# Optimization experiments

Measured on AMD Instinct MI355X. Metric: run time of the kernel, lower is better.

## Reference

```python
import jax, jax.numpy as jnp
import numpy as np

N, E, IN_DIM, H, EDGE_DIM, T, SCALE = 50000, 800000, 16, 32, 4, 4, 3

def setup_inputs() -> dict:
    key = jax.random.key(0)
    ks = jax.random.split(key, 12)
    s = 0.1
    return {
        "inputs": jax.random.normal(ks[0], (N, IN_DIM), jnp.float32),
        "e_feats": jax.random.normal(ks[1], (E, EDGE_DIM, T), jnp.float32),
        "rain0": jax.random.uniform(ks[2], (N, T), jnp.float32),
        "W_emb": jax.random.normal(ks[3], (IN_DIM, H), jnp.float32) * s,
        "W_edge_in": jax.random.normal(ks[4], (SCALE - 1, H + EDGE_DIM, H), jnp.float32) * s,
        "W_node_in": jax.random.normal(ks[5], (SCALE - 1, 2 * H + 1, H), jnp.float32) * s,
        "W_edge_out": jax.random.normal(ks[6], (H + EDGE_DIM, H), jnp.float32) * s,
        "W_node_out": jax.random.normal(ks[7], (2 * H + 1, H), jnp.float32) * s,
        "W_rain": jax.random.normal(ks[8], (H, 1), jnp.float32) * s,
        "src": jax.random.randint(ks[9], (E,), 0, N, jnp.int32),
        "dst": jax.random.randint(ks[10], (E,), 0, N, jnp.int32),
    }


def _eiconv(h, ef, rain, W_e, W_n, src, dst):
    # edge-conditioned message: act_edge(W_e @ [h_src ; e_feat])  -> [E, H]
    m = jax.nn.relu(jnp.concatenate([h[src], ef], axis=-1) @ W_e)
    # scatter-sum to destination nodes  -> [N, H]
    agg = jax.ops.segment_sum(m, dst, num_segments=h.shape[0])
    # node update conditioned on rain driver: act_o(W_n @ [h ; agg ; rain])
    return jax.nn.relu(jnp.concatenate([h, agg, rain[:, None]], axis=-1) @ W_n)


def reference(inputs, e_feats, rain0, W_emb, W_edge_in, W_node_in, W_edge_out, W_node_out, W_rain, src, dst):
    h0 = inputs @ W_emb  # embedding, no bias  [N, H]
    ef_t = jnp.transpose(e_feats, (2, 0, 1))  # [T, E, edge_dim]
    rain_t = rain0.T  # [T, N]

    def step(h, xs):
        ef, rain = xs
        for s in range(SCALE - 1):  # IN layers (fixed small loop)
            h = _eiconv(h, ef, rain, W_edge_in[s], W_node_in[s], src, dst)
        h = _eiconv(h, ef, rain, W_edge_out, W_node_out, src, dst)  # OUT layer
        r = (h @ W_rain)[:, 0]  # per-node rain scalar
        return h, r

    _, rains = jax.lax.scan(step, h0, (ef_t, rain_t))  # rains: [T, N]
    return rains.T  # rain_all: [N, T]
```

## Files before the change

kernel.cpp:

```cpp
#include <hip/hip_runtime.h>
#include <cstdint>

#define NN 50000
#define NE 800000
#define IN_DIM 16
#define H 32
#define EDGE_DIM 4
#define T_STEPS 4
#define NPB 32
#define NBLK ((NN + NPB - 1) / NPB)
#define SBLK 196

typedef __bf16 bf16x8 __attribute__((ext_vector_type(8)));
typedef float f32x4 __attribute__((ext_vector_type(4)));
typedef unsigned int u32x4 __attribute__((ext_vector_type(4)));

__device__ __forceinline__ uint32_t bf_rne1(float f) {
    uint32_t u = __float_as_uint(f);
    return (u + 0x7FFFu + ((u >> 16) & 1u)) >> 16;
}
__device__ __forceinline__ float bf2f(uint32_t h16) { return __uint_as_float(h16 << 16); }
__device__ __forceinline__ uint32_t bfpair(float a, float b) {
    return (bf_rne1(b) << 16) | bf_rne1(a);
}
__device__ __forceinline__ bf16x8 asbf(u32x4 u) { return __builtin_bit_cast(bf16x8, u); }
__device__ __forceinline__ f32x4 MFMA(bf16x8 a, bf16x8 b, f32x4 c) {
    return __builtin_amdgcn_mfma_f32_16x16x32_bf16(a, b, c, 0, 0, 0);
}

__device__ __forceinline__ void store_hpk(uint32_t* hpk, int n, int cq, float4 a) {
    int off = (cq & 3) * 4 + (cq >> 2) * 2;
    uint32_t p0 = bfpair(a.x, a.y), p1 = bfpair(a.z, a.w);
    *(uint2*)(hpk + (size_t)n * 32 + off) = make_uint2(p0, p1);
    float r0 = a.x - bf2f(p0 & 0xFFFFu), r1 = a.y - bf2f(p0 >> 16);
    float r2 = a.z - bf2f(p1 & 0xFFFFu), r3 = a.w - bf2f(p1 >> 16);
    *(uint2*)(hpk + (size_t)n * 32 + 16 + off) = make_uint2(bfpair(r0, r1), bfpair(r2, r3));
}

__global__ __launch_bounds__(256) void embed_kernel(const float* __restrict__ inputs,
                                                    const float* __restrict__ W_emb,
                                                    float* __restrict__ h,
                                                    uint32_t* __restrict__ hpk) {
    int idx = blockIdx.x * 256 + threadIdx.x;
    if (idx >= NN * 8) return;
    int n = idx >> 3, cq = idx & 7;
    const float* xr = inputs + (size_t)n * IN_DIM;
    float4 a = make_float4(0.f, 0.f, 0.f, 0.f);
#pragma unroll
    for (int k = 0; k < IN_DIM; ++k) {
        float xk = xr[k];
        float4 w = *(const float4*)(W_emb + k * 32 + cq * 4);
        a.x = fmaf(xk, w.x, a.x); a.y = fmaf(xk, w.y, a.y);
        a.z = fmaf(xk, w.z, a.z); a.w = fmaf(xk, w.w, a.w);
    }
    *(float4*)(h + (size_t)n * 32 + cq * 4) = a;
    store_hpk(hpk, n, cq, a);
}

__global__ __launch_bounds__(256) void hist_kernel(const int* __restrict__ dst, int* __restrict__ deg) {
    int e = blockIdx.x * 256 + threadIdx.x;
    if (e < NE) atomicAdd(&deg[dst[e]], 1);
}

__global__ __launch_bounds__(256) void scan_part(const int* __restrict__ deg, int* __restrict__ bsum) {
    __shared__ int red[256];
    int i = blockIdx.x * 256 + threadIdx.x;
    red[threadIdx.x] = (i < NN) ? deg[i] : 0;
    __syncthreads();
    for (int off = 128; off > 0; off >>= 1) {
        if (threadIdx.x < off) red[threadIdx.x] += red[threadIdx.x + off];
        __syncthreads();
    }
    if (threadIdx.x == 0) bsum[blockIdx.x] = red[0];
}

__global__ __launch_bounds__(256) void scan_tops(const int* __restrict__ bsum, int* __restrict__ btop) {
    __shared__ int s[256];
    int tid = threadIdx.x;
    int v0 = (tid < SBLK) ? bsum[tid] : 0;
    s[tid] = v0;
    __syncthreads();
    for (int off = 1; off < 256; off <<= 1) {
        int v = (tid >= off) ? s[tid - off] : 0;
        __syncthreads();
        s[tid] += v;
        __syncthreads();
    }
    if (tid < SBLK) btop[tid] = s[tid] - v0;
}

__global__ __launch_bounds__(256) void scan_final(const int* __restrict__ deg,
                                                  const int* __restrict__ btop,
                                                  int* __restrict__ row_ptr) {
    __shared__ int s[256];
    int tid = threadIdx.x;
    int i = blockIdx.x * 256 + tid;
    int v0 = (i < NN) ? deg[i] : 0;
    s[tid] = v0;
    __syncthreads();
    for (int off = 1; off < 256; off <<= 1) {
        int v = (tid >= off) ? s[tid - off] : 0;
        __syncthreads();
        s[tid] += v;
        __syncthreads();
    }
    if (i <= NN) row_ptr[i] = btop[blockIdx.x] + s[tid] - v0;
}

__global__ __launch_bounds__(256) void scatter_kernel(const int* __restrict__ src, const int* __restrict__ dst,
                                                      const int* __restrict__ row_ptr, int* __restrict__ cnt,
                                                      uint2* __restrict__ se_sorted) {
    int e = blockIdx.x * 256 + threadIdx.x;
    if (e >= NE) return;
    int d = dst[e];
    int pos = row_ptr[d] + atomicAdd(&cnt[d], 1);
    se_sorted[pos] = make_uint2((unsigned)src[e], (unsigned)e);
}

__global__ __launch_bounds__(256) void ef_sort_kernel(const float* __restrict__ e_feats,
                                                      const uint2* __restrict__ se_sorted,
                                                      u32x4* __restrict__ ef4) {
    int p = blockIdx.x * 256 + threadIdx.x;
    if (p >= NE) return;
    int e = (int)se_sorted[p].y;
    float buf[16];
    const float4* srcp = (const float4*)(e_feats + (size_t)e * (EDGE_DIM * T_STEPS));
#pragma unroll
    for (int q = 0; q < 4; ++q) {
        float4 v = srcp[q];
        buf[4 * q + 0] = v.x; buf[4 * q + 1] = v.y; buf[4 * q + 2] = v.z; buf[4 * q + 3] = v.w;
    }
#pragma unroll
    for (int t = 0; t < T_STEPS; ++t) {
        float f0 = buf[t], f1 = buf[4 + t], f2 = buf[8 + t], f3 = buf[12 + t];
        uint32_t h0 = bfpair(f0, f1), h1 = bfpair(f2, f3);
        float r0 = f0 - bf2f(h0 & 0xFFFFu), r1 = f1 - bf2f(h0 >> 16);
        float r2 = f2 - bf2f(h1 & 0xFFFFu), r3 = f3 - bf2f(h1 >> 16);
        u32x4 o = {h0, h1, bfpair(r0, r1), bfpair(r2, r3)};
        ef4[(size_t)t * NE + p] = o;
    }
}

__global__ __launch_bounds__(256) void wefrag_kernel(const float* __restrict__ We_in,
                                                     const float* __restrict__ We_out,
                                                     u32x4* __restrict__ frag) {
    int idx = blockIdx.x * 256 + threadIdx.x;
    if (idx >= 3 * 2 * 2 * 2 * 64) return;
    int lane = idx & 63;
    int hl = (idx >> 6) & 1;
    int nt = (idx >> 7) & 1;
    int ks = (idx >> 8) & 1;
    int mat = idx >> 9;
    const float* W = (mat < 2) ? (We_in + (size_t)mat * 36 * 32) : We_out;
    int col = (lane & 15) + nt * 16;
    int kb = ks * 32 + ((lane >> 4) & 3) * 4;
    u32x4 o;
#pragma unroll
    for (int i = 0; i < 4; ++i) {
        int k0 = kb + (i >= 2 ? 16 : 0) + (i & 1) * 2;
        float v0 = (k0 < 36) ? W[(size_t)k0 * 32 + col] : 0.f;
        float v1 = (k0 + 1 < 36) ? W[(size_t)(k0 + 1) * 32 + col] : 0.f;
        if (hl) {
            v0 -= bf2f(bf_rne1(v0));
            v1 -= bf2f(bf_rne1(v1));
        }
        o[i] = bfpair(v0, v1);
    }
    frag[idx] = o;
}

__global__ __launch_bounds__(256) void layer_kernel(const float* __restrict__ h,
                                                    const uint32_t* __restrict__ hpk,
                                                    const u32x4* __restrict__ ef4,
                                                    const uint2* __restrict__ se,
                                                    const int* __restrict__ row_ptr,
                                                    const float* __restrict__ rain0,
                                                    const u32x4* __restrict__ wfrag,
                                                    const float* __restrict__ Wn,
                                                    const float* __restrict__ Wrain,
                                                    float* __restrict__ hnew,
                                                    uint32_t* __restrict__ hnpk,
                                                    float* __restrict__ out,
                                                    int t, int last) {
    __shared__ float msg[4][2][16 * 36];
    __shared__ float shl[NPB * 36];
    __shared__ float sagg[NPB * 36];

    int tid = threadIdx.x;
    int lane = tid & 63, w = tid >> 6;
    int nb0 = blockIdx.x * NPB;
    int l15 = lane & 15, kg = lane >> 4;

    int rpv = row_ptr[min(nb0 + w * 8 + min(lane, 8), NN)];
    int e0w = __shfl(rpv, 0);
    int e1w = __shfl(rpv, 8);
    int sg = lane >> 3, sl = lane & 7;
    int arb = __shfl(rpv, sg);
    int are = __shfl(rpv, sg + 1);

    {
        int nl = w * 8 + sg;
        int n = nb0 + nl;
        if (n < NN)
            *(float4*)&shl[nl * 36 + sl * 4] = *(const float4*)(h + (size_t)n * 32 + sl * 4);
    }

    u32x4 b[2][2][2];
#pragma unroll
    for (int ks = 0; ks < 2; ++ks)
#pragma unroll
        for (int nt = 0; nt < 2; ++nt)
#pragma unroll
            for (int hl = 0; hl < 2; ++hl)
                b[ks][nt][hl] = wfrag[((ks * 2 + nt) * 2 + hl) * 64 + lane];

    float4 aggv = make_float4(0.f, 0.f, 0.f, 0.f);
    float* msgW0 = &msg[w][0][0];
    float* msgW1 = &msg[w][1][0];

    struct Frag { u32x4 ah, al, e4; };

    auto loadFrag = [&](int i) -> Frag {
        Frag f;
        int p = e0w + i * 16 + l15;
        int pc = p < e1w ? p : e1w - 1;
        int s = (int)se[pc].x;
        const u32x4* hp = (const u32x4*)(hpk + (size_t)s * 32);
        f.ah = hp[kg];
        f.al = hp[4 + kg];
        f.e4 = (kg == 0) ? ef4[pc] : u32x4{0u, 0u, 0u, 0u};
        return f;
    };
    auto compute = [&](Frag f, float* msgW) {
        u32x4 a1h = {f.e4[0], f.e4[1], 0u, 0u};
        u32x4 a1l = {f.e4[2], f.e4[3], 0u, 0u};
        f32x4 c0 = {0.f, 0.f, 0.f, 0.f};
        f32x4 c1 = {0.f, 0.f, 0.f, 0.f};
        bf16x8 Ah = asbf(f.ah), Al = asbf(f.al), Eh = asbf(a1h), El = asbf(a1l);
        c0 = MFMA(Ah, asbf(b[0][0][0]), c0);
        c0 = MFMA(Ah, asbf(b[0][0][1]), c0);
        c0 = MFMA(Al, asbf(b[0][0][0]), c0);
        c0 = MFMA(Eh, asbf(b[1][0][0]), c0);
        c0 = MFMA(Eh, asbf(b[1][0][1]), c0);
        c0 = MFMA(El, asbf(b[1][0][0]), c0);
        c1 = MFMA(Ah, asbf(b[0][1][0]), c1);
        c1 = MFMA(Ah, asbf(b[0][1][1]), c1);
        c1 = MFMA(Al, asbf(b[0][1][0]), c1);
        c1 = MFMA(Eh, asbf(b[1][1][0]), c1);
        c1 = MFMA(Eh, asbf(b[1][1][1]), c1);
        c1 = MFMA(El, asbf(b[1][1][0]), c1);
#pragma unroll
        for (int r = 0; r < 4; ++r) {
            msgW[(kg * 4 + r) * 36 + l15] = fmaxf(c0[r], 0.f);
            msgW[(kg * 4 + r) * 36 + 16 + l15] = fmaxf(c1[r], 0.f);
        }
    };
    auto segsum = [&](int i, const float* msgW) {
        int tb = e0w + i * 16;
        int lo = max(arb, tb), hi2 = min(are, tb + 16);
        for (int p2 = lo; p2 < hi2; ++p2) {
            float4 v = *(const float4*)&msgW[(p2 - tb) * 36 + sl * 4];
            aggv.x += v.x; aggv.y += v.y; aggv.z += v.z; aggv.w += v.w;
        }
    };

    if (e1w > e0w) {
        int nT = (e1w - e0w + 15) >> 4;
        Frag f0 = loadFrag(0);
        Frag f1 = loadFrag(1);
#pragma unroll 1
        for (int i = 0; i < nT; ++i) {
            Frag fn = loadFrag(i + 2);
            float* mw = (i & 1) ? msgW1 : msgW0;
            compute(f0, mw);
            segsum(i, mw);
            f0 = f1; f1 = fn;
        }
    }
    {
        int nl = w * 8 + sg;
        *(float4*)&sagg[nl * 36 + sl * 4] = aggv;
    }

    int nl = w * 8 + sg;
    int n = nb0 + nl;
    if (n < NN) {
        float4 a = make_float4(0.f, 0.f, 0.f, 0.f);
#pragma unroll 8
        for (int k = 0; k < 32; ++k) {
            float xk = shl[nl * 36 + k];
            float4 wv = *(const float4*)(Wn + (size_t)k * 32 + sl * 4);
            a.x = fmaf(xk, wv.x, a.x); a.y = fmaf(xk, wv.y, a.y);
            a.z = fmaf(xk, wv.z, a.z); a.w = fmaf(xk, wv.w, a.w);
        }
#pragma unroll 8
        for (int k = 0; k < 32; ++k) {
            float xk = sagg[nl * 36 + k];
            float4 wv = *(const float4*)(Wn + (size_t)(32 + k) * 32 + sl * 4);
            a.x = fmaf(xk, wv.x, a.x); a.y = fmaf(xk, wv.y, a.y);
            a.z = fmaf(xk, wv.z, a.z); a.w = fmaf(xk, wv.w, a.w);
        }
        {
            float rain = rain0[(size_t)n * T_STEPS + t];
            float4 wv = *(const float4*)(Wn + (size_t)64 * 32 + sl * 4);
            a.x = fmaf(rain, wv.x, a.x); a.y = fmaf(rain, wv.y, a.y);
            a.z = fmaf(rain, wv.z, a.z); a.w = fmaf(rain, wv.w, a.w);
        }
        a.x = fmaxf(a.x, 0.f); a.y = fmaxf(a.y, 0.f);
        a.z = fmaxf(a.z, 0.f); a.w = fmaxf(a.w, 0.f);
        *(float4*)(hnew + (size_t)n * 32 + sl * 4) = a;
        store_hpk(hnpk, n, sl, a);
        if (last) {
            float4 wr = *(const float4*)(Wrain + sl * 4);
            float rv = a.x * wr.x + a.y * wr.y + a.z * wr.z + a.w * wr.w;
            rv += __shfl_xor(rv, 1);
            rv += __shfl_xor(rv, 2);
            rv += __shfl_xor(rv, 4);
            if (sl == 0) out[(size_t)n * T_STEPS + t] = rv;
        }
    }
}

extern "C" void kernel_launch(void* const* d_in, const int* in_sizes, int n_in,
                              void* d_out, int out_size, void* d_ws, size_t ws_size,
                              hipStream_t stream) {
    const float* inputs     = (const float*)d_in[0];
    const float* e_feats    = (const float*)d_in[1];
    const float* rain0      = (const float*)d_in[2];
    const float* W_emb      = (const float*)d_in[3];
    const float* W_edge_in  = (const float*)d_in[4];
    const float* W_node_in  = (const float*)d_in[5];
    const float* W_edge_out = (const float*)d_in[6];
    const float* W_node_out = (const float*)d_in[7];
    const float* W_rain     = (const float*)d_in[8];
    const int*   src        = (const int*)d_in[9];
    const int*   dst        = (const int*)d_in[10];
    float* out = (float*)d_out;

    float* h_a = (float*)d_ws;
    float* h_b = h_a + (size_t)NN * 32;
    uint32_t* hpk_a = (uint32_t*)(h_b + (size_t)NN * 32);
    uint32_t* hpk_b = hpk_a + (size_t)NN * 32;
    u32x4* ef4      = (u32x4*)(hpk_b + (size_t)NN * 32);
    u32x4* wfrag    = ef4 + (size_t)T_STEPS * NE;
    int* row_ptr    = (int*)(wfrag + 1536);
    int* deg        = row_ptr + (NN + 1);
    int* cnt        = deg + NN;
    uint2* se       = (uint2*)(cnt + NN + 1);
    int* bsum       = (int*)(se + NE);
    int* btop       = bsum + SBLK;

    embed_kernel<<<(NN * 8 + 255) / 256, 256, 0, stream>>>(inputs, W_emb, h_a, hpk_a);

    hipMemsetAsync(deg, 0, (size_t)2 * NN * sizeof(int), stream);
    hist_kernel<<<(NE + 255) / 256, 256, 0, stream>>>(dst, deg);
    scan_part<<<SBLK, 256, 0, stream>>>(deg, bsum);
    scan_tops<<<1, 256, 0, stream>>>(bsum, btop);
    scan_final<<<SBLK, 256, 0, stream>>>(deg, btop, row_ptr);
    scatter_kernel<<<(NE + 255) / 256, 256, 0, stream>>>(src, dst, row_ptr, cnt, se);
    ef_sort_kernel<<<(NE + 255) / 256, 256, 0, stream>>>(e_feats, se, ef4);
    wefrag_kernel<<<6, 256, 0, stream>>>(W_edge_in, W_edge_out, wfrag);

    float* hc = h_a;  float* hn = h_b;
    uint32_t* pkc = hpk_a; uint32_t* pkn = hpk_b;
    for (int t = 0; t < T_STEPS; ++t) {
        const u32x4* ef4_t = ef4 + (size_t)t * NE;
        for (int s = 0; s < 3; ++s) {
            int mat = (s < 2) ? s : 2;
            const float* Wn = (s < 2) ? (W_node_in + (size_t)s * 65 * 32) : W_node_out;
            layer_kernel<<<NBLK, 256, 0, stream>>>(hc, pkc, ef4_t, se, row_ptr, rain0,
                                                   wfrag + (size_t)mat * 512, Wn, W_rain,
                                                   hn, pkn, out, t, (s == 2) ? 1 : 0);
            float* tf = hc; hc = hn; hn = tf;
            uint32_t* tp = pkc; pkc = pkn; pkn = tp;
        }
    }
}
```

Measured before the change: 633.2 us.

## Replace LDS segment-sum with MFMA selection-matrix reduction over 16 nodes per wave

The per-edge messages no longer go through shared memory for a serial per-node summation loop. Instead they are split into bf16 hi/lo pairs and reduced into destination nodes with MFMA against a 0/1 selection matrix built from row_ptr ranges. Each wave now handles 16 nodes and NPB doubles to 64, which halves the block count and processes 32 edges per iteration. This removes LDS round-trips and divergent variable-length loops. In exchange it adds conversion ALU work and extra MFMAs, and it may lower parallelism and change occupancy.

```diff
diff --git a/kernel.cpp b/kernel.cpp
--- a/kernel.cpp
+++ b/kernel.cpp
@@ -7,7 +7,7 @@
 #define H 32
 #define EDGE_DIM 4
 #define T_STEPS 4
-#define NPB 32
+#define NPB 64
 #define NBLK ((NN + NPB - 1) / NPB)
 #define SBLK 196
 
@@ -26,6 +26,18 @@
 __device__ __forceinline__ bf16x8 asbf(u32x4 u) { return __builtin_bit_cast(bf16x8, u); }
 __device__ __forceinline__ f32x4 MFMA(bf16x8 a, bf16x8 b, f32x4 c) {
     return __builtin_amdgcn_mfma_f32_16x16x32_bf16(a, b, c, 0, 0, 0);
+}
+__device__ __forceinline__ uint32_t cvt_pk_bf16(float a, float b) {
+    uint32_t r;
+    asm("v_cvt_pk_bf16_f32 %0, %1, %2" : "=v"(r) : "v"(a), "v"(b));
+    return r;
+}
+__device__ __forceinline__ uint2 split_pair(float m0, float m1) {
+    uint32_t hi = cvt_pk_bf16(m0, m1);
+    float h0 = __uint_as_float(hi << 16);
+    float h1 = __uint_as_float(hi & 0xFFFF0000u);
+    uint32_t lo = cvt_pk_bf16(m0 - h0, m1 - h1);
+    return make_uint2(hi, lo);
 }
 
 __device__ __forceinline__ void store_hpk(uint32_t* hpk, int n, int cq, float4 a) {
@@ -182,27 +194,28 @@
                                                     uint32_t* __restrict__ hnpk,
                                                     float* __restrict__ out,
                                                     int t, int last) {
-    __shared__ float msg[4][2][16 * 36];
     __shared__ float shl[NPB * 36];
     __shared__ float sagg[NPB * 36];
 
     int tid = threadIdx.x;
     int lane = tid & 63, w = tid >> 6;
     int nb0 = blockIdx.x * NPB;
+    int nbw = nb0 + w * 16;
     int l15 = lane & 15, kg = lane >> 4;
 
-    int rpv = row_ptr[min(nb0 + w * 8 + min(lane, 8), NN)];
+    int rpv = row_ptr[min(nbw + min(lane, 16), NN)];
     int e0w = __shfl(rpv, 0);
-    int e1w = __shfl(rpv, 8);
-    int sg = lane >> 3, sl = lane & 7;
-    int arb = __shfl(rpv, sg);
-    int are = __shfl(rpv, sg + 1);
-
-    {
-        int nl = w * 8 + sg;
+    int e1w = __shfl(rpv, 16);
+    int arb = __shfl(rpv, l15);
+    int are = __shfl(rpv, l15 + 1);
+
+#pragma unroll
+    for (int it = 0; it < 2; ++it) {
+        int idx = it * 64 + lane;
+        int nl = w * 16 + (idx >> 3), q = idx & 7;
         int n = nb0 + nl;
         if (n < NN)
-            *(float4*)&shl[nl * 36 + sl * 4] = *(const float4*)(h + (size_t)n * 32 + sl * 4);
+            *(float4*)&shl[nl * 36 + q * 4] = *(const float4*)(h + (size_t)n * 32 + q * 4);
     }
 
     u32x4 b[2][2][2];
@@ -214,12 +227,7 @@
             for (int hl = 0; hl < 2; ++hl)
                 b[ks][nt][hl] = wfrag[((ks * 2 + nt) * 2 + hl) * 64 + lane];
 
-    float4 aggv = make_float4(0.f, 0.f, 0.f, 0.f);
-    float* msgW0 = &msg[w][0][0];
-    float* msgW1 = &msg[w][1][0];
-
     struct Frag { u32x4 ah, al, e4; };
-
     auto loadFrag = [&](int i) -> Frag {
         Frag f;
         int p = e0w + i * 16 + l15;
@@ -231,11 +239,9 @@
         f.e4 = (kg == 0) ? ef4[pc] : u32x4{0u, 0u, 0u, 0u};
         return f;
     };
-    auto compute = [&](Frag f, float* msgW) {
+    auto computeMsg = [&](Frag f, f32x4& c0, f32x4& c1) {
         u32x4 a1h = {f.e4[0], f.e4[1], 0u, 0u};
         u32x4 a1l = {f.e4[2], f.e4[3], 0u, 0u};
-        f32x4 c0 = {0.f, 0.f, 0.f, 0.f};
-        f32x4 c1 = {0.f, 0.f, 0.f, 0.f};
         bf16x8 Ah = asbf(f.ah), Al = asbf(f.al), Eh = asbf(a1h), El = asbf(a1l);
         c0 = MFMA(Ah, asbf(b[0][0][0]), c0);
         c0 = MFMA(Ah, asbf(b[0][0][1]), c0);
@@ -249,74 +255,103 @@
         c1 = MFMA(Eh, asbf(b[1][1][0]), c1);
         c1 = MFMA(Eh, asbf(b[1][1][1]), c1);
         c1 = MFMA(El, asbf(b[1][1][0]), c1);
-#pragma unroll
-        for (int r = 0; r < 4; ++r) {
-            msgW[(kg * 4 + r) * 36 + l15] = fmaxf(c0[r], 0.f);
-            msgW[(kg * 4 + r) * 36 + 16 + l15] = fmaxf(c1[r], 0.f);
+    };
+
+    f32x4 aggD0 = {0.f, 0.f, 0.f, 0.f};
+    f32x4 aggD1 = {0.f, 0.f, 0.f, 0.f};
+    int kb4 = kg * 4;
+
+    if (e1w > e0w) {
+        int nP = (e1w - e0w + 31) >> 5;
+        Frag fa0 = loadFrag(0), fb0 = loadFrag(1);
+        Frag fa1 = loadFrag(2), fb1 = loadFrag(3);
+#pragma unroll 1
+        for (int i = 0; i < nP; ++i) {
+            Frag fan = loadFrag((i + 2) * 2);
+            Frag fbn = loadFrag((i + 2) * 2 + 1);
+            f32x4 c0A = {0.f,0.f,0.f,0.f}, c1A = {0.f,0.f,0.f,0.f};
+            f32x4 c0B = {0.f,0.f,0.f,0.f}, c1B = {0.f,0.f,0.f,0.f};
+            computeMsg(fa0, c0A, c1A);
+            computeMsg(fb0, c0B, c1B);
+#pragma unroll
+            for (int r = 0; r < 4; ++r) {
+                c0A[r] = fmaxf(c0A[r], 0.f); c1A[r] = fmaxf(c1A[r], 0.f);
+                c0B[r] = fmaxf(c0B[r], 0.f); c1B[r] = fmaxf(c1B[r], 0.f);
+            }
+            u32x4 Bh0, Bl0, Bh1, Bl1;
+            uint2 sp;
+            sp = split_pair(c0A[0], c0A[1]); Bh0[0] = sp.x; Bl0[0] = sp.y;
+            sp = split_pair(c0A[2], c0A[3]); Bh0[1] = sp.x; Bl0[1] = sp.y;
+            sp = split_pair(c0B[0], c0B[1]); Bh0[2] = sp.x; Bl0[2] = sp.y;
+            sp = split_pair(c0B[2], c0B[3]); Bh0[3] = sp.x; Bl0[3] = sp.y;
+            sp = split_pair(c1A[0], c1A[1]); Bh1[0] = sp.x; Bl1[0] = sp.y;
+            sp = split_pair(c1A[2], c1A[3]); Bh1[1] = sp.x; Bl1[1] = sp.y;
+            sp = split_pair(c1B[0], c1B[1]); Bh1[2] = sp.x; Bl1[2] = sp.y;
+            sp = split_pair(c1B[2], c1B[3]); Bh1[3] = sp.x; Bl1[3] = sp.y;
+            int tb = e0w + i * 32;
+            u32x4 S;
+#pragma unroll
+            for (int j = 0; j < 4; ++j) {
+                int k0 = kb4 + (j & 1) * 2 + ((j >= 2) ? 16 : 0);
+                int p0 = tb + k0, p1 = p0 + 1;
+                uint32_t s0 = ((unsigned)(p0 - arb) < (unsigned)(are - arb)) ? 0x3F80u : 0u;
+                uint32_t s1 = ((unsigned)(p1 - arb) < (unsigned)(are - arb)) ? 0x3F800000u : 0u;
+                S[j] = s0 | s1;
+            }
+            bf16x8 selA = asbf(S);
+            aggD0 = MFMA(selA, asbf(Bh0), aggD0);
+            aggD0 = MFMA(selA, asbf(Bl0), aggD0);
+            aggD1 = MFMA(selA, asbf(Bh1), aggD1);
+            aggD1 = MFMA(selA, asbf(Bl1), aggD1);
+            fa0 = fa1; fb0 = fb1; fa1 = fan; fb1 = fbn;
         }
-    };
-    auto segsum = [&](int i, const float* msgW) {
-        int tb = e0w + i * 16;
-        int lo = max(arb, tb), hi2 = min(are, tb + 16);
-        for (int p2 = lo; p2 < hi2; ++p2) {
-            float4 v = *(const float4*)&msgW[(p2 - tb) * 36 + sl * 4];
-            aggv.x += v.x; aggv.y += v.y; aggv.z += v.z; aggv.w += v.w;
-        }
-    };
-
-    if (e1w > e0w) {
-        int nT = (e1w - e0w + 15) >> 4;
-        Frag f0 = loadFrag(0);
-        Frag f1 = loadFrag(1);
-#pragma unroll 1
-        for (int i = 0; i < nT; ++i) {
-            Frag fn = loadFrag(i + 2);
-            float* mw = (i & 1) ? msgW1 : msgW0;
-            compute(f0, mw);
-            segsum(i, mw);
-            f0 = f1; f1 = fn;
-        }
-    }
-    {
-        int nl = w * 8 + sg;
-        *(float4*)&sagg[nl * 36 + sl * 4] = aggv;
-    }
-
-    int nl = w * 8 + sg;
-    int n = nb0 + nl;
-    if (n < NN) {
-        float4 a = make_float4(0.f, 0.f, 0.f, 0.f);
+    }
+#pragma unroll
+    for (int r = 0; r < 4; ++r) {
+        int nl = w * 16 + kg * 4 + r;
+        sagg[nl * 36 + l15] = aggD0[r];
+        sagg[nl * 36 + 16 + l15] = aggD1[r];
+    }
+
+    int sg = lane >> 3, sl = lane & 7;
+#pragma unroll
+    for (int pass = 0; pass < 2; ++pass) {
+        int nl = w * 16 + pass * 8 + sg;
+        int n = nb0 + nl;
+        if (n < NN) {
+            float4 a = make_float4(0.f, 0.f, 0.f, 0.f);
 #pragma unroll 8
-        for (int k = 0; k < 32; ++k) {
-            float xk = shl[nl * 36 + k];
-            float4 wv = *(const float4*)(Wn + (size_t)k * 32 + sl * 4);
-            a.x = fmaf(xk, wv.x, a.x); a.y = fmaf(xk, wv.y, a.y);
-            a.z = fmaf(xk, wv.z, a.z); a.w = fmaf(xk, wv.w, a.w);
-        }
+            for (int k = 0; k < 32; ++k) {
+                float xk = shl[nl * 36 + k];
+                float4 wv = *(const float4*)(Wn + (size_t)k * 32 + sl * 4);
+                a.x = fmaf(xk, wv.x, a.x); a.y = fmaf(xk, wv.y, a.y);
+                a.z = fmaf(xk, wv.z, a.z); a.w = fmaf(xk, wv.w, a.w);
+            }
 #pragma unroll 8
-        for (int k = 0; k < 32; ++k) {
-            float xk = sagg[nl * 36 + k];
-            float4 wv = *(const float4*)(Wn + (size_t)(32 + k) * 32 + sl * 4);
-            a.x = fmaf(xk, wv.x, a.x); a.y = fmaf(xk, wv.y, a.y);
-            a.z = fmaf(xk, wv.z, a.z); a.w = fmaf(xk, wv.w, a.w);
-        }
-        {
-            float rain = rain0[(size_t)n * T_STEPS + t];
-            float4 wv = *(const float4*)(Wn + (size_t)64 * 32 + sl * 4);
-            a.x = fmaf(rain, wv.x, a.x); a.y = fmaf(rain, wv.y, a.y);
-            a.z = fmaf(rain, wv.z, a.z); a.w = fmaf(rain, wv.w, a.w);
-        }
-        a.x = fmaxf(a.x, 0.f); a.y = fmaxf(a.y, 0.f);
-        a.z = fmaxf(a.z, 0.f); a.w = fmaxf(a.w, 0.f);
-        *(float4*)(hnew + (size_t)n * 32 + sl * 4) = a;
-        store_hpk(hnpk, n, sl, a);
-        if (last) {
-            float4 wr = *(const float4*)(Wrain + sl * 4);
-            float rv = a.x * wr.x + a.y * wr.y + a.z * wr.z + a.w * wr.w;
-            rv += __shfl_xor(rv, 1);
-            rv += __shfl_xor(rv, 2);
-            rv += __shfl_xor(rv, 4);
-            if (sl == 0) out[(size_t)n * T_STEPS + t] = rv;
+            for (int k = 0; k < 32; ++k) {
+                float xk = sagg[nl * 36 + k];
+                float4 wv = *(const float4*)(Wn + (size_t)(32 + k) * 32 + sl * 4);
+                a.x = fmaf(xk, wv.x, a.x); a.y = fmaf(xk, wv.y, a.y);
+                a.z = fmaf(xk, wv.z, a.z); a.w = fmaf(xk, wv.w, a.w);
+            }
+            {
+                float rain = rain0[(size_t)n * T_STEPS + t];
+                float4 wv = *(const float4*)(Wn + (size_t)64 * 32 + sl * 4);
+                a.x = fmaf(rain, wv.x, a.x); a.y = fmaf(rain, wv.y, a.y);
+                a.z = fmaf(rain, wv.z, a.z); a.w = fmaf(rain, wv.w, a.w);
+            }
+            a.x = fmaxf(a.x, 0.f); a.y = fmaxf(a.y, 0.f);
+            a.z = fmaxf(a.z, 0.f); a.w = fmaxf(a.w, 0.f);
+            *(float4*)(hnew + (size_t)n * 32 + sl * 4) = a;
+            store_hpk(hnpk, n, sl, a);
+            if (last) {
+                float4 wr = *(const float4*)(Wrain + sl * 4);
+                float rv = a.x * wr.x + a.y * wr.y + a.z * wr.z + a.w * wr.w;
+                rv += __shfl_xor(rv, 1);
+                rv += __shfl_xor(rv, 2);
+                rv += __shfl_xor(rv, 4);
+                if (sl == 0) out[(size_t)n * T_STEPS + t] = rv;
+            }
         }
     }
 }
```

New measurement: 724.3 us. 1.14x slower.
